# Kernel optimization log

Hardware: AMD Instinct MI355X
Metric: run time of the kernel (lower is better)

The kernel has to match this reference:

```python
import jax, jax.numpy as jnp
import numpy as np

N = 100000   # nodes
E = 1600000  # edges (avg degree 16)
IN, H, OUT = 256, 256, 40


def setup_inputs() -> dict:
    key = jax.random.key(0)
    ks = jax.random.split(key, 10)
    x = jax.random.normal(ks[0], (N, IN), dtype=jnp.float32)
    edge_index = jax.random.randint(ks[1], (2, E), 0, N, dtype=jnp.int32)
    def lin_init(k, fan_in, fan_out):
        s = 1.0 / np.sqrt(fan_in)
        kw, kb = jax.random.split(k)
        W = jax.random.uniform(kw, (fan_in, fan_out), jnp.float32, -s, s)
        b = jax.random.uniform(kb, (fan_out,), jnp.float32, -s, s)
        return W, b
    W1, b1 = lin_init(ks[2], IN, H)
    W2, b2 = lin_init(ks[3], H, H)
    W3, b3 = lin_init(ks[4], H, OUT)
    lin_w, lin_b = lin_init(ks[5], 2 * H + OUT, OUT)  # skip-concat projection
    return {"x": x, "edge_index": edge_index, "W1": W1, "b1": b1,
            "W2": W2, "b2": b2, "W3": W3, "b3": b3,
            "lin_w": lin_w, "lin_b": lin_b}


def reference(x, edge_index, W1, b1, W2, b2, W3, b3, lin_w, lin_b):
    n = x.shape[0]
    loops = jnp.arange(n, dtype=edge_index.dtype)
    row = jnp.concatenate([edge_index[0], loops])  # source nodes
    col = jnp.concatenate([edge_index[1], loops])  # target nodes
    # GCN symmetric normalization (deg includes self-loops, so deg >= 1)
    deg = jax.ops.segment_sum(jnp.ones_like(col, dtype=x.dtype), col, num_segments=n)
    dis = jax.lax.rsqrt(deg)
    norm = (dis[row] * dis[col])[:, None]

    def gcn(h, W, b):
        h = h @ W  # transform first, then propagate (PyG GCNConv)
        agg = jax.ops.segment_sum(h[row] * norm, col, num_segments=n)
        return agg + b

    h1 = jax.nn.relu(gcn(x, W1, b1))   # dropout p=0 -> identity
    h2 = jax.nn.relu(gcn(h1, W2, b2))
    h3 = jax.nn.relu(gcn(h2, W3, b3))
    out = jnp.concatenate([h1, h2, h3], axis=-1) @ lin_w + lin_b
    return jax.nn.log_softmax(out, axis=1)
```

## Files before the change

kernel.cpp:

```cpp
#include <hip/hip_runtime.h>
#include <math.h>

typedef unsigned short u16;
typedef unsigned int u32;
typedef unsigned char u8;
typedef __attribute__((ext_vector_type(8))) short bf16x8;
typedef __attribute__((ext_vector_type(4))) float f32x4;
typedef __attribute__((ext_vector_type(2))) float f32x2;

#define CAP 64

__device__ __forceinline__ float bf2f(u16 u) {
    union { unsigned u; float f; } v; v.u = (unsigned)u << 16; return v.f;
}
__device__ __forceinline__ u16 f2bf(float f) {
    union { float f; unsigned u; } v; v.f = f;
    unsigned r = v.u + 0x7FFF + ((v.u >> 16) & 1);
    return (u16)(r >> 16);
}


__global__ void mega_fused(const int* __restrict__ erow, const int* __restrict__ ecol,
                           int* __restrict__ cnt, int* __restrict__ srcs,
                           int e, int chunk, int FB,
                           const float* __restrict__ W1, const float* __restrict__ W2,
                           const float* __restrict__ W3, const float* __restrict__ lw,
                           u16* __restrict__ W1t, u16* __restrict__ W2t,
                           u16* __restrict__ W3t, u16* __restrict__ lwAt,
                           u16* __restrict__ lwBt, u16* __restrict__ lwCt) {
    int b = blockIdx.x;
    if (b < FB) {
        int w = b & 7;
        int rank = b >> 3;
        int cohortThreads = (FB >> 3) * 256;
        int t0 = rank * 256 + threadIdx.x;
        int lo = w * chunk, hi = lo + chunk;
        for (int i = t0; i < e; i += cohortThreads) {
            int c = __builtin_nontemporal_load(&ecol[i]);
            if (c >= lo && c < hi) {
                int r = __builtin_nontemporal_load(&erow[i]);
                int slot = atomicAdd(&cnt[c], 1);
                if (slot < CAP) srcs[(size_t)c * CAP + slot] = r;
            }
        }
    } else {
        int idx = (b - FB) * 256 + threadIdx.x;
        if (idx < 65536) {
            int n = idx >> 8, k = idx & 255;
            W1t[idx] = f2bf(W1[k * 256 + n]);
        } else if (idx < 131072) {
            int i = idx - 65536; int n = i >> 8, k = i & 255;
            W2t[i] = f2bf(W2[k * 256 + n]);
        } else if (idx < 163840) {
            int i = idx - 131072; int n = i >> 8, k = i & 255;
            W3t[i] = (n < 40) ? f2bf(W3[k * 40 + n]) : (u16)0;
        } else if (idx < 196608) {
            int i = idx - 163840; int n = i >> 8, k = i & 255;
            lwAt[i] = (n < 40) ? f2bf(lw[k * 40 + n]) : (u16)0;
        } else if (idx < 229376) {
            int i = idx - 196608; int n = i >> 8, k = i & 255;
            lwBt[i] = (n < 40) ? f2bf(lw[(256 + k) * 40 + n]) : (u16)0;
        } else if (idx < 237568) {
            int i = idx - 229376; int n = i >> 6, k = i & 63;
            lwCt[i] = (n < 40 && k < 40) ? f2bf(lw[(512 + k) * 40 + n]) : (u16)0;
        }
    }
}

__global__ void dis_kernel(const int* __restrict__ cnt, float* __restrict__ dis, int n) {
    int i = blockIdx.x * blockDim.x + threadIdx.x;
    if (i < n) dis[i] = rsqrtf((float)cnt[i] + 1.0f);
}


#define SWZ(row) ((((row) & 3) ^ (((row) >> 2) & 3)))

__device__ __forceinline__ void gload_lds16(const void* g, void* l) {
    __builtin_amdgcn_global_load_lds(
        (const __attribute__((address_space(1))) unsigned int*)g,
        (__attribute__((address_space(3))) unsigned int*)l, 16, 0, 0);
}


__global__ __launch_bounds__(512) void gemm256_x32(
    const float* __restrict__ A, int lda,
    const u16* __restrict__ Bt, int ldb,
    u8* __restrict__ C,
    int M, int K)
{
    __shared__ u16 As[128 * 32];
    __shared__ u16 Bs[256 * 32];
    int tid = threadIdx.x;
    int ln = tid & 63, wv = tid >> 6;
    int wr = wv >> 2, wc = wv & 3;
    int br = blockIdx.y * 128;

    f32x4 acc[4][4];
    #pragma unroll
    for (int m = 0; m < 4; ++m)
        #pragma unroll
        for (int n = 0; n < 4; ++n)
            acc[m][n] = (f32x4){0.f, 0.f, 0.f, 0.f};

    for (int k0 = 0; k0 < K; k0 += 32) {
        __syncthreads();
        {
            int row = tid >> 2, sp = tid & 3;
            int sl = sp ^ SWZ(row);
            int arow = br + row; if (arow >= M) arow = M - 1;
            const float* ga = A + (size_t)arow * lda + k0 + sl * 8;
            float4 v0 = *(const float4*)ga;
            float4 v1 = *(const float4*)(ga + 4);
            bf16x8 pk;
            pk[0] = (short)f2bf(v0.x); pk[1] = (short)f2bf(v0.y);
            pk[2] = (short)f2bf(v0.z); pk[3] = (short)f2bf(v0.w);
            pk[4] = (short)f2bf(v1.x); pk[5] = (short)f2bf(v1.y);
            pk[6] = (short)f2bf(v1.z); pk[7] = (short)f2bf(v1.w);
            *(bf16x8*)((char*)As + row * 64 + sp * 16) = pk;
        }
        #pragma unroll
        for (int r = 0; r < 2; ++r) {
            int l = r * 512 + tid;
            int row = l >> 2, sp = l & 3;
            int sl = sp ^ SWZ(row);
            gload_lds16(Bt + (size_t)row * ldb + k0 + sl * 8,
                        (char*)Bs + r * 8192 + wv * 1024);
        }
        __syncthreads();
        bf16x8 af[4], bf_[4];
        #pragma unroll
        for (int m = 0; m < 4; ++m) {
            int row = wr * 64 + m * 16 + (ln & 15);
            int sl = ((ln >> 4) ^ SWZ(row)) & 3;
            af[m] = *(const bf16x8*)((const char*)As + row * 64 + sl * 16);
        }
        #pragma unroll
        for (int n = 0; n < 4; ++n) {
            int row = wc * 64 + n * 16 + (ln & 15);
            int sl = ((ln >> 4) ^ SWZ(row)) & 3;
            bf_[n] = *(const bf16x8*)((const char*)Bs + row * 64 + sl * 16);
        }
        #pragma unroll
        for (int m = 0; m < 4; ++m)
            #pragma unroll
            for (int n = 0; n < 4; ++n)
                acc[m][n] = __builtin_amdgcn_mfma_f32_16x16x32_bf16(af[m], bf_[n], acc[m][n], 0, 0, 0);
    }

    #pragma unroll
    for (int m = 0; m < 4; ++m) {
        #pragma unroll
        for (int n = 0; n < 4; ++n) {
            #pragma unroll
            for (int j = 0; j < 4; ++j) {
                int r = br + wr * 64 + m * 16 + (ln >> 4) * 4 + j;
                int c = wc * 64 + n * 16 + (ln & 15);
                if (r < M) {
                    float v = acc[m][n][j];
                    u32 pk = __builtin_amdgcn_cvt_pk_fp8_f32(v, v, 0, false);
                    C[(size_t)r * 256 + c] = (u8)(pk & 0xff);
                }
            }
        }
    }
}


__global__ __launch_bounds__(512) void gemm256(
    const u16* __restrict__ A, int lda,
    const u16* __restrict__ Bt, int ldb,
    u8* __restrict__ C,
    int M, int K)
{
    __shared__ u16 As[128 * 32];
    __shared__ u16 Bs[256 * 32];
    int tid = threadIdx.x;
    int ln = tid & 63, wv = tid >> 6;
    int wr = wv >> 2, wc = wv & 3;
    int br = blockIdx.y * 128;

    f32x4 acc[4][4];
    #pragma unroll
    for (int m = 0; m < 4; ++m)
        #pragma unroll
        for (int n = 0; n < 4; ++n)
            acc[m][n] = (f32x4){0.f, 0.f, 0.f, 0.f};

    for (int k0 = 0; k0 < K; k0 += 32) {
        __syncthreads();
        {
            int l = tid;
            int row = l >> 2, sp = l & 3;
            int sl = sp ^ SWZ(row);
            int arow = br + row; if (arow >= M) arow = M - 1;
            gload_lds16(A + (size_t)arow * lda + k0 + sl * 8,
                        (char*)As + wv * 1024);
        }
        #pragma unroll
        for (int r = 0; r < 2; ++r) {
            int l = r * 512 + tid;
            int row = l >> 2, sp = l & 3;
            int sl = sp ^ SWZ(row);
            gload_lds16(Bt + (size_t)row * ldb + k0 + sl * 8,
                        (char*)Bs + r * 8192 + wv * 1024);
        }
        __syncthreads();
        bf16x8 af[4], bf_[4];
        #pragma unroll
        for (int m = 0; m < 4; ++m) {
            int row = wr * 64 + m * 16 + (ln & 15);
            int sl = ((ln >> 4) ^ SWZ(row)) & 3;
            af[m] = *(const bf16x8*)((const char*)As + row * 64 + sl * 16);
        }
        #pragma unroll
        for (int n = 0; n < 4; ++n) {
            int row = wc * 64 + n * 16 + (ln & 15);
            int sl = ((ln >> 4) ^ SWZ(row)) & 3;
            bf_[n] = *(const bf16x8*)((const char*)Bs + row * 64 + sl * 16);
        }
        #pragma unroll
        for (int m = 0; m < 4; ++m)
            #pragma unroll
            for (int n = 0; n < 4; ++n)
                acc[m][n] = __builtin_amdgcn_mfma_f32_16x16x32_bf16(af[m], bf_[n], acc[m][n], 0, 0, 0);
    }

    #pragma unroll
    for (int m = 0; m < 4; ++m) {
        #pragma unroll
        for (int n = 0; n < 4; ++n) {
            #pragma unroll
            for (int j = 0; j < 4; ++j) {
                int r = br + wr * 64 + m * 16 + (ln >> 4) * 4 + j;
                int c = wc * 64 + n * 16 + (ln & 15);
                if (r < M) {
                    float v = acc[m][n][j];
                    u32 pk = __builtin_amdgcn_cvt_pk_fp8_f32(v, v, 0, false);
                    C[(size_t)r * 256 + c] = (u8)(pk & 0xff);
                }
            }
        }
    }
}


__global__ __launch_bounds__(256) void gemm_w3(
    const u16* __restrict__ A, int lda,
    const u16* __restrict__ Bt, int ldb,
    u8* __restrict__ C,
    int M, int K)
{
    __shared__ u16 As[128 * 32];
    __shared__ u16 Bs[64 * 32];
    int tid = threadIdx.x;
    int ln = tid & 63, wv = tid >> 6;
    int br = blockIdx.y * 128;

    f32x4 acc[2][4];
    #pragma unroll
    for (int m = 0; m < 2; ++m)
        #pragma unroll
        for (int n = 0; n < 4; ++n)
            acc[m][n] = (f32x4){0.f, 0.f, 0.f, 0.f};

    for (int k0 = 0; k0 < K; k0 += 32) {
        __syncthreads();
        #pragma unroll
        for (int r = 0; r < 2; ++r) {
            int l = r * 256 + tid;
            int row = l >> 2, sp = l & 3;
            int sl = sp ^ SWZ(row);
            int arow = br + row; if (arow >= M) arow = M - 1;
            gload_lds16(A + (size_t)arow * lda + k0 + sl * 8,
                        (char*)As + r * 4096 + wv * 1024);
        }
        {
            int l = tid;
            int row = l >> 2, sp = l & 3;
            int sl = sp ^ SWZ(row);
            gload_lds16(Bt + (size_t)row * ldb + k0 + sl * 8,
                        (char*)Bs + wv * 1024);
        }
        __syncthreads();
        bf16x8 af[2], bf_[4];
        #pragma unroll
        for (int m = 0; m < 2; ++m) {
            int row = wv * 32 + m * 16 + (ln & 15);
            int sl = ((ln >> 4) ^ SWZ(row)) & 3;
            af[m] = *(const bf16x8*)((const char*)As + row * 64 + sl * 16);
        }
        #pragma unroll
        for (int n = 0; n < 4; ++n) {
            int row = n * 16 + (ln & 15);
            int sl = ((ln >> 4) ^ SWZ(row)) & 3;
            bf_[n] = *(const bf16x8*)((const char*)Bs + row * 64 + sl * 16);
        }
        #pragma unroll
        for (int m = 0; m < 2; ++m)
            #pragma unroll
            for (int n = 0; n < 4; ++n)
                acc[m][n] = __builtin_amdgcn_mfma_f32_16x16x32_bf16(af[m], bf_[n], acc[m][n], 0, 0, 0);
    }

    #pragma unroll
    for (int m = 0; m < 2; ++m) {
        #pragma unroll
        for (int n = 0; n < 4; ++n) {
            #pragma unroll
            for (int j = 0; j < 4; ++j) {
                int r = br + wv * 32 + m * 16 + (ln >> 4) * 4 + j;
                int c = n * 16 + (ln & 15);
                if (r < M) {
                    float v = acc[m][n][j];
                    u32 pk = __builtin_amdgcn_cvt_pk_fp8_f32(v, v, 0, false);
                    C[(size_t)r * 64 + c] = (u8)(pk & 0xff);
                }
            }
        }
    }
}


__global__ __launch_bounds__(256) void gemm3_lsm(
    const u16* __restrict__ A0, const u16* __restrict__ A1, const u16* __restrict__ A2,
    const u16* __restrict__ B0, const u16* __restrict__ B1, const u16* __restrict__ B2,
    const float* __restrict__ bias,
    float* __restrict__ out, int M)
{
    __shared__ u16 As[128 * 32];
    __shared__ u16 Bs[64 * 32];
    int tid = threadIdx.x;
    int ln = tid & 63, wv = tid >> 6;
    int br = blockIdx.x * 128;

    f32x4 acc[2][4];
    #pragma unroll
    for (int m = 0; m < 2; ++m)
        #pragma unroll
        for (int n = 0; n < 4; ++n)
            acc[m][n] = (f32x4){0.f, 0.f, 0.f, 0.f};

    auto do_seg = [&](const u16* __restrict__ A, const u16* __restrict__ B, int K) {
        for (int k0 = 0; k0 < K; k0 += 32) {
            __syncthreads();
            #pragma unroll
            for (int r = 0; r < 2; ++r) {
                int l = r * 256 + tid;
                int row = l >> 2, sp = l & 3;
                int sl = sp ^ SWZ(row);
                int arow = br + row; if (arow >= M) arow = M - 1;
                gload_lds16(A + (size_t)arow * K + k0 + sl * 8,
                            (char*)As + r * 4096 + wv * 1024);
            }
            {
                int l = tid;
                int row = l >> 2, sp = l & 3;
                int sl = sp ^ SWZ(row);
                gload_lds16(B + (size_t)row * K + k0 + sl * 8,
                            (char*)Bs + wv * 1024);
            }
            __syncthreads();
            bf16x8 af[2], bf_[4];
            #pragma unroll
            for (int m = 0; m < 2; ++m) {
                int row = wv * 32 + m * 16 + (ln & 15);
                int sl = ((ln >> 4) ^ SWZ(row)) & 3;
                af[m] = *(const bf16x8*)((const char*)As + row * 64 + sl * 16);
            }
            #pragma unroll
            for (int nn = 0; nn < 4; ++nn) {
                int row = nn * 16 + (ln & 15);
                int sl = ((ln >> 4) ^ SWZ(row)) & 3;
                bf_[nn] = *(const bf16x8*)((const char*)Bs + row * 64 + sl * 16);
            }
            #pragma unroll
            for (int m = 0; m < 2; ++m)
                #pragma unroll
                for (int nn = 0; nn < 4; ++nn)
                    acc[m][nn] = __builtin_amdgcn_mfma_f32_16x16x32_bf16(af[m], bf_[nn], acc[m][nn], 0, 0, 0);
        }
    };
    do_seg(A0, B0, 256);
    do_seg(A1, B1, 256);
    do_seg(A2, B2, 64);

    int l15 = ln & 15;
    #pragma unroll
    for (int m = 0; m < 2; ++m) {
        #pragma unroll
        for (int j = 0; j < 4; ++j) {
            int r = br + wv * 32 + m * 16 + (ln >> 4) * 4 + j;
            float v0 = acc[m][0][j] + bias[l15];
            float v1 = acc[m][1][j] + bias[16 + l15];
            float v2 = (l15 < 8) ? (acc[m][2][j] + bias[32 + l15]) : -INFINITY;
            float mx = fmaxf(fmaxf(v0, v1), v2);
            #pragma unroll
            for (int o = 8; o; o >>= 1) mx = fmaxf(mx, __shfl_xor(mx, o));
            float s = expf(v0 - mx) + expf(v1 - mx) + ((l15 < 8) ? expf(v2 - mx) : 0.f);
            #pragma unroll
            for (int o = 8; o; o >>= 1) s += __shfl_xor(s, o);
            float ls = logf(s);
            if (r < M) {
                out[(size_t)r * 40 + l15]      = v0 - mx - ls;
                out[(size_t)r * 40 + 16 + l15] = v1 - mx - ls;
                if (l15 < 8) out[(size_t)r * 40 + 32 + l15] = v2 - mx - ls;
            }
        }
    }
}


__global__ __launch_bounds__(256) void agg256_fp8(
    const u8* __restrict__ ht,
    const int* __restrict__ cnt,
    const int* __restrict__ srcs, const float* __restrict__ dis,
    const float* __restrict__ bias,
    u16* __restrict__ outb, int n)
{
    int wv = threadIdx.x >> 6, ln = threadIdx.x & 63;
    int i = blockIdx.x * 4 + wv;
    if (i >= n) return;
    int c = ln * 4;
    float di = dis[i], dd = di * di;
    u32 sv = *(const u32*)(ht + (size_t)i * 256 + c);
    f32x2 slo = __builtin_amdgcn_cvt_pk_f32_fp8(sv, false);
    f32x2 shi = __builtin_amdgcn_cvt_pk_f32_fp8(sv, true);
    float a0 = slo[0] * dd, a1 = slo[1] * dd, a2 = shi[0] * dd, a3 = shi[1] * dd;
    int beg = i * CAP;
    int num = cnt[i]; if (num > CAP) num = CAP;
    {
        int sl = 0; float dsl = 0.f;
        if (ln < num) { sl = srcs[beg + ln]; dsl = dis[sl]; }
        int j = 0;
        for (; j + 8 <= num; j += 8) {
            int s[8]; float w[8]; u32 v[8];
            #pragma unroll
            for (int q = 0; q < 8; ++q) {
                s[q] = __shfl(sl, j + q);
                w[q] = __shfl(dsl, j + q) * di;
            }
            #pragma unroll
            for (int q = 0; q < 8; ++q)
                v[q] = *(const u32*)(ht + (size_t)s[q] * 256 + c);
            #pragma unroll
            for (int q = 0; q < 8; ++q) {
                f32x2 lo = __builtin_amdgcn_cvt_pk_f32_fp8(v[q], false);
                f32x2 hi = __builtin_amdgcn_cvt_pk_f32_fp8(v[q], true);
                a0 += lo[0] * w[q]; a1 += lo[1] * w[q];
                a2 += hi[0] * w[q]; a3 += hi[1] * w[q];
            }
        }
        for (; j + 4 <= num; j += 4) {
            int s[4]; float w[4]; u32 v[4];
            #pragma unroll
            for (int q = 0; q < 4; ++q) {
                s[q] = __shfl(sl, j + q);
                w[q] = __shfl(dsl, j + q) * di;
            }
            #pragma unroll
            for (int q = 0; q < 4; ++q)
                v[q] = *(const u32*)(ht + (size_t)s[q] * 256 + c);
            #pragma unroll
            for (int q = 0; q < 4; ++q) {
                f32x2 lo = __builtin_amdgcn_cvt_pk_f32_fp8(v[q], false);
                f32x2 hi = __builtin_amdgcn_cvt_pk_f32_fp8(v[q], true);
                a0 += lo[0] * w[q]; a1 += lo[1] * w[q];
                a2 += hi[0] * w[q]; a3 += hi[1] * w[q];
            }
        }
        for (; j < num; ++j) {
            int s0 = __shfl(sl, j);
            float w0 = __shfl(dsl, j) * di;
            u32 v0 = *(const u32*)(ht + (size_t)s0 * 256 + c);
            f32x2 lo = __builtin_amdgcn_cvt_pk_f32_fp8(v0, false);
            f32x2 hi = __builtin_amdgcn_cvt_pk_f32_fp8(v0, true);
            a0 += lo[0] * w0; a1 += lo[1] * w0;
            a2 += hi[0] * w0; a3 += hi[1] * w0;
        }
    }
    float4 bv = *(const float4*)(bias + c);
    ushort4 o;
    o.x = f2bf(fmaxf(a0 + bv.x, 0.f));
    o.y = f2bf(fmaxf(a1 + bv.y, 0.f));
    o.z = f2bf(fmaxf(a2 + bv.z, 0.f));
    o.w = f2bf(fmaxf(a3 + bv.w, 0.f));
    *(ushort4*)(outb + (size_t)i * 256 + c) = o;
}

__global__ __launch_bounds__(256) void agg40_fp8(
    const u8* __restrict__ ht,
    const int* __restrict__ cnt,
    const int* __restrict__ srcs, const float* __restrict__ dis,
    const float* __restrict__ bias,
    u16* __restrict__ outb, int n)
{
    int half = threadIdx.x >> 5;
    int l = threadIdx.x & 31;
    int i = blockIdx.x * 8 + half;
    if (i >= n) return;
    int c2 = l * 2;
    float di = dis[i], dd = di * di;
    u32 sv = (u32)*(const u16*)(ht + (size_t)i * 64 + c2);
    f32x2 sf = __builtin_amdgcn_cvt_pk_f32_fp8(sv, false);
    float a0 = sf[0] * dd, a1 = sf[1] * dd;
    int beg = i * CAP;
    int num = cnt[i]; if (num > CAP) num = CAP;
    for (int base = 0; base < num; base += 32) {
        int rem = num - base; if (rem > 32) rem = 32;
        int sl = 0; float dsl = 0.f;
        if (l < rem) { sl = srcs[beg + base + l]; dsl = dis[sl]; }
        int j = 0;
        for (; j + 8 <= rem; j += 8) {
            int s[8]; float w[8]; u32 v[8];
            #pragma unroll
            for (int q = 0; q < 8; ++q) {
                s[q] = __shfl(sl, j + q, 32);
                w[q] = __shfl(dsl, j + q, 32) * di;
            }
            #pragma unroll
            for (int q = 0; q < 8; ++q)
                v[q] = (u32)*(const u16*)(ht + (size_t)s[q] * 64 + c2);
            #pragma unroll
            for (int q = 0; q < 8; ++q) {
                f32x2 f = __builtin_amdgcn_cvt_pk_f32_fp8(v[q], false);
                a0 += f[0] * w[q]; a1 += f[1] * w[q];
            }
        }
        for (; j + 4 <= rem; j += 4) {
            int s[4]; float w[4]; u32 v[4];
            #pragma unroll
            for (int q = 0; q < 4; ++q) {
                s[q] = __shfl(sl, j + q, 32);
                w[q] = __shfl(dsl, j + q, 32) * di;
            }
            #pragma unroll
            for (int q = 0; q < 4; ++q)
                v[q] = (u32)*(const u16*)(ht + (size_t)s[q] * 64 + c2);
            #pragma unroll
            for (int q = 0; q < 4; ++q) {
                f32x2 f = __builtin_amdgcn_cvt_pk_f32_fp8(v[q], false);
                a0 += f[0] * w[q]; a1 += f[1] * w[q];
            }
        }
        for (; j < rem; ++j) {
            int s0 = __shfl(sl, j, 32);
            float w0 = __shfl(dsl, j, 32) * di;
            u32 v0 = (u32)*(const u16*)(ht + (size_t)s0 * 64 + c2);
            f32x2 f = __builtin_amdgcn_cvt_pk_f32_fp8(v0, false);
            a0 += f[0] * w0; a1 += f[1] * w0;
        }
    }
    u32 o;
    if (l < 20) {
        float b0 = bias[c2], b1 = bias[c2 + 1];
        o = (u32)f2bf(fmaxf(a0 + b0, 0.f)) | ((u32)f2bf(fmaxf(a1 + b1, 0.f)) << 16);
    } else {
        o = 0u;
    }
    *(u32*)(outb + (size_t)i * 64 + c2) = o;
}


extern "C" void kernel_launch(void* const* d_in, const int* in_sizes, int n_in,
                              void* d_out, int out_size, void* d_ws, size_t ws_size,
                              hipStream_t stream)
{
    const float* x  = (const float*)d_in[0];
    const int*   ei = (const int*)d_in[1];
    const float* W1 = (const float*)d_in[2];
    const float* b1 = (const float*)d_in[3];
    const float* W2 = (const float*)d_in[4];
    const float* b2 = (const float*)d_in[5];
    const float* W3 = (const float*)d_in[6];
    const float* b3 = (const float*)d_in[7];
    const float* lw = (const float*)d_in[8];
    const float* lb = (const float*)d_in[9];

    int N = in_sizes[0] / 256;
    int E = in_sizes[1] / 2;
    const int* erow = ei;
    const int* ecol = ei + E;

    char* ws = (char*)d_ws;
    size_t o = 0;
    auto alloc = [&](size_t bytes) -> void* {
        void* p = ws + o;
        o += (bytes + 255) & ~(size_t)255;
        return p;
    };
    int*   cnt  = (int*)alloc((size_t)N * 4);
    float* dis  = (float*)alloc((size_t)N * 4);
    int*   srcs = (int*)alloc((size_t)N * CAP * 4);
    u16*   W1t  = (u16*)alloc(256 * 256 * 2);
    u16*   W2t  = (u16*)alloc(256 * 256 * 2);
    u16*   W3t  = (u16*)alloc(128 * 256 * 2);
    u16*   lwAt = (u16*)alloc(128 * 256 * 2);
    u16*   lwBt = (u16*)alloc(128 * 256 * 2);
    u16*   lwCt = (u16*)alloc(128 * 64 * 2);
    u8*    htb  = (u8*)alloc((size_t)N * 256 * 2);
    u16*   h1b  = (u16*)alloc((size_t)N * 256 * 2);
    u16*   h2b  = (u16*)alloc((size_t)N * 256 * 2);
    u16*   h3b  = (u16*)alloc((size_t)N * 64 * 2);
    u8*    ht3b = htb;

    const int tb = 256;

    hipMemsetAsync(cnt, 0, (size_t)N * 4, stream);
    const int FB = 2048;
    int PB = (237568 + tb - 1) / tb;
    int chunk = (N + 7) / 8;
    mega_fused<<<FB + PB, tb, 0, stream>>>(
        erow, ecol, cnt, srcs, E, chunk, FB,
        W1, W2, W3, lw, W1t, W2t, W3t, lwAt, lwBt, lwCt);

    dis_kernel<<<(N + tb - 1) / tb, tb, 0, stream>>>(cnt, dis, N);

    dim3 gBig(1, (N + 127) / 128);
    int nAgg4 = (N + 3) / 4;
    int nAgg8 = (N + 7) / 8;

    gemm256_x32<<<gBig, 512, 0, stream>>>(x, 256, W1t, 256, htb, N, 256);
    agg256_fp8<<<nAgg4, 256, 0, stream>>>(htb, cnt, srcs, dis, b1, h1b, N);
    gemm256<<<gBig, 512, 0, stream>>>(h1b, 256, W2t, 256, htb, N, 256);
    agg256_fp8<<<nAgg4, 256, 0, stream>>>(htb, cnt, srcs, dis, b2, h2b, N);
    gemm_w3<<<gBig, 256, 0, stream>>>(h2b, 256, W3t, 256, ht3b, N, 256);
    agg40_fp8<<<nAgg8, 256, 0, stream>>>(ht3b, cnt, srcs, dis, b3, h3b, N);

    gemm3_lsm<<<(N + 127) / 128, 256, 0, stream>>>(
        h1b, h2b, h3b, lwAt, lwBt, lwCt, lb, (float*)d_out, N);
}
```

Baseline: 353.9 us.

## Fuse edge bucketing with first GEMM in interleaved-block kernel

Moves the weight transpose and bf16 conversion into its own small kernel. The atomic edge-bucketing fill and the first-layer x·W1 GEMM now share one launch, with blocks interleaved so memory- and atomic-bound fill work runs alongside the MFMA GEMM. Fill blocks now use 512 threads, with half as many blocks, so the total thread count is unchanged. The cost is that fill blocks also reserve the GEMM's LDS, which can lower occupancy, and weight prep adds a separate launch ahead of the fused kernel.

```diff
diff --git a/kernel.cpp b/kernel.cpp
--- a/kernel.cpp
+++ b/kernel.cpp
@@ -19,21 +19,72 @@
     return (u16)(r >> 16);
 }
 
-
-__global__ void mega_fused(const int* __restrict__ erow, const int* __restrict__ ecol,
-                           int* __restrict__ cnt, int* __restrict__ srcs,
-                           int e, int chunk, int FB,
-                           const float* __restrict__ W1, const float* __restrict__ W2,
-                           const float* __restrict__ W3, const float* __restrict__ lw,
-                           u16* __restrict__ W1t, u16* __restrict__ W2t,
-                           u16* __restrict__ W3t, u16* __restrict__ lwAt,
-                           u16* __restrict__ lwBt, u16* __restrict__ lwCt) {
+__global__ void prep_weights(const float* __restrict__ W1, const float* __restrict__ W2,
+                             const float* __restrict__ W3, const float* __restrict__ lw,
+                             u16* __restrict__ W1t, u16* __restrict__ W2t,
+                             u16* __restrict__ W3t, u16* __restrict__ lwAt,
+                             u16* __restrict__ lwBt, u16* __restrict__ lwCt) {
+    int idx = blockIdx.x * blockDim.x + threadIdx.x;
+    if (idx < 65536) {
+        int n = idx >> 8, k = idx & 255;
+        W1t[idx] = f2bf(W1[k * 256 + n]);
+    } else if (idx < 131072) {
+        int i = idx - 65536; int n = i >> 8, k = i & 255;
+        W2t[i] = f2bf(W2[k * 256 + n]);
+    } else if (idx < 163840) {
+        int i = idx - 131072; int n = i >> 8, k = i & 255;
+        W3t[i] = (n < 40) ? f2bf(W3[k * 40 + n]) : (u16)0;
+    } else if (idx < 196608) {
+        int i = idx - 163840; int n = i >> 8, k = i & 255;
+        lwAt[i] = (n < 40) ? f2bf(lw[k * 40 + n]) : (u16)0;
+    } else if (idx < 229376) {
+        int i = idx - 196608; int n = i >> 8, k = i & 255;
+        lwBt[i] = (n < 40) ? f2bf(lw[(256 + k) * 40 + n]) : (u16)0;
+    } else if (idx < 237568) {
+        int i = idx - 229376; int n = i >> 6, k = i & 63;
+        lwCt[i] = (n < 40 && k < 40) ? f2bf(lw[(512 + k) * 40 + n]) : (u16)0;
+    }
+}
+
+__global__ void dis_kernel(const int* __restrict__ cnt, float* __restrict__ dis, int n) {
+    int i = blockIdx.x * blockDim.x + threadIdx.x;
+    if (i < n) dis[i] = rsqrtf((float)cnt[i] + 1.0f);
+}
+
+
+#define SWZ(row) ((((row) & 3) ^ (((row) >> 2) & 3)))
+
+__device__ __forceinline__ void gload_lds16(const void* g, void* l) {
+    __builtin_amdgcn_global_load_lds(
+        (const __attribute__((address_space(1))) unsigned int*)g,
+        (__attribute__((address_space(3))) unsigned int*)l, 16, 0, 0);
+}
+
+
+__global__ __launch_bounds__(512) void fill_gemm1(
+    const int* __restrict__ erow, const int* __restrict__ ecol,
+    int* __restrict__ cnt, int* __restrict__ srcs, int e, int chunk, int FB, int GB,
+    const float* __restrict__ A, int lda,
+    const u16* __restrict__ Bt, int ldb,
+    u8* __restrict__ C, int M, int K)
+{
+    __shared__ u16 As[128 * 32];
+    __shared__ u16 Bs[256 * 32];
     int b = blockIdx.x;
-    if (b < FB) {
-        int w = b & 7;
-        int rank = b >> 3;
-        int cohortThreads = (FB >> 3) * 256;
-        int t0 = rank * 256 + threadIdx.x;
+    int fidx, gidx;
+    if (b < 2 * GB) {
+        if (b & 1) { fidx = b >> 1; gidx = -1; }
+        else       { gidx = b >> 1; fidx = -1; }
+    } else {
+        fidx = GB + (b - 2 * GB);
+        gidx = -1;
+    }
+
+    if (fidx >= 0) {
+        int w = fidx & 7;
+        int rank = fidx >> 3;
+        int cohortThreads = (FB >> 3) * 512;
+        int t0 = rank * 512 + threadIdx.x;
         int lo = w * chunk, hi = lo + chunk;
         for (int i = t0; i < e; i += cohortThreads) {
             int c = __builtin_nontemporal_load(&ecol[i]);
@@ -43,57 +94,13 @@
                 if (slot < CAP) srcs[(size_t)c * CAP + slot] = r;
             }
         }
-    } else {
-        int idx = (b - FB) * 256 + threadIdx.x;
-        if (idx < 65536) {
-            int n = idx >> 8, k = idx & 255;
-            W1t[idx] = f2bf(W1[k * 256 + n]);
-        } else if (idx < 131072) {
-            int i = idx - 65536; int n = i >> 8, k = i & 255;
-            W2t[i] = f2bf(W2[k * 256 + n]);
-        } else if (idx < 163840) {
-            int i = idx - 131072; int n = i >> 8, k = i & 255;
-            W3t[i] = (n < 40) ? f2bf(W3[k * 40 + n]) : (u16)0;
-        } else if (idx < 196608) {
-            int i = idx - 163840; int n = i >> 8, k = i & 255;
-            lwAt[i] = (n < 40) ? f2bf(lw[k * 40 + n]) : (u16)0;
-        } else if (idx < 229376) {
-            int i = idx - 196608; int n = i >> 8, k = i & 255;
-            lwBt[i] = (n < 40) ? f2bf(lw[(256 + k) * 40 + n]) : (u16)0;
-        } else if (idx < 237568) {
-            int i = idx - 229376; int n = i >> 6, k = i & 63;
-            lwCt[i] = (n < 40 && k < 40) ? f2bf(lw[(512 + k) * 40 + n]) : (u16)0;
-        }
-    }
-}
-
-__global__ void dis_kernel(const int* __restrict__ cnt, float* __restrict__ dis, int n) {
-    int i = blockIdx.x * blockDim.x + threadIdx.x;
-    if (i < n) dis[i] = rsqrtf((float)cnt[i] + 1.0f);
-}
-
-
-#define SWZ(row) ((((row) & 3) ^ (((row) >> 2) & 3)))
-
-__device__ __forceinline__ void gload_lds16(const void* g, void* l) {
-    __builtin_amdgcn_global_load_lds(
-        (const __attribute__((address_space(1))) unsigned int*)g,
-        (__attribute__((address_space(3))) unsigned int*)l, 16, 0, 0);
-}
-
-
-__global__ __launch_bounds__(512) void gemm256_x32(
-    const float* __restrict__ A, int lda,
-    const u16* __restrict__ Bt, int ldb,
-    u8* __restrict__ C,
-    int M, int K)
-{
-    __shared__ u16 As[128 * 32];
-    __shared__ u16 Bs[256 * 32];
+        return;
+    }
+
     int tid = threadIdx.x;
     int ln = tid & 63, wv = tid >> 6;
     int wr = wv >> 2, wc = wv & 3;
-    int br = blockIdx.y * 128;
+    int br = gidx * 128;
 
     f32x4 acc[4][4];
     #pragma unroll
@@ -606,12 +613,15 @@
     const int tb = 256;
 
     hipMemsetAsync(cnt, 0, (size_t)N * 4, stream);
-    const int FB = 2048;
-    int PB = (237568 + tb - 1) / tb;
+    prep_weights<<<(237568 + tb - 1) / tb, tb, 0, stream>>>(
+        W1, W2, W3, lw, W1t, W2t, W3t, lwAt, lwBt, lwCt);
+
+    const int FB = 1024;
+    int GB = (N + 127) / 128;
     int chunk = (N + 7) / 8;
-    mega_fused<<<FB + PB, tb, 0, stream>>>(
-        erow, ecol, cnt, srcs, E, chunk, FB,
-        W1, W2, W3, lw, W1t, W2t, W3t, lwAt, lwBt, lwCt);
+    fill_gemm1<<<FB + GB, 512, 0, stream>>>(
+        erow, ecol, cnt, srcs, E, chunk, FB, GB,
+        x, 256, W1t, 256, htb, N, 256);
 
     dis_kernel<<<(N + tb - 1) / tb, tb, 0, stream>>>(cnt, dis, N);
 
@@ -619,7 +629,6 @@
     int nAgg4 = (N + 3) / 4;
     int nAgg8 = (N + 7) / 8;
 
-    gemm256_x32<<<gBig, 512, 0, stream>>>(x, 256, W1t, 256, htb, N, 256);
     agg256_fp8<<<nAgg4, 256, 0, stream>>>(htb, cnt, srcs, dis, b1, h1b, N);
     gemm256<<<gBig, 512, 0, stream>>>(h1b, 256, W2t, 256, htb, N, 256);
     agg256_fp8<<<nAgg4, 256, 0, stream>>>(htb, cnt, srcs, dis, b2, h2b, N);
```

Measured after the change: 419.5 us. 18.5% more time.
